# Kernel optimization log

Hardware: AMD Instinct MI355X
Metric: run time of the kernel (lower is better)

The kernel has to match this reference:

```python
import jax, jax.numpy as jnp
import numpy as np

MARGIN = 0.3
IN_FEATURES = 128
NUM_CLASSES = 100
BATCH = 4096


def setup_inputs() -> dict:
    key = jax.random.key(0)
    k1, k2, k3, k4 = jax.random.split(key, 4)
    embeddings = jax.random.normal(k1, (BATCH, IN_FEATURES), dtype=jnp.float32)
    labels = jax.random.randint(k2, (BATCH,), 0, NUM_CLASSES, dtype=jnp.int64)
    # nn.Linear params (kaiming-uniform-ish scale)
    bound = 1.0 / np.sqrt(IN_FEATURES)
    fc_w = jax.random.uniform(k3, (NUM_CLASSES, IN_FEATURES), jnp.float32, -bound, bound)
    fc_b = jax.random.uniform(k4, (NUM_CLASSES,), jnp.float32, -bound, bound)
    return {"embeddings": embeddings, "labels": labels, "fc_w": fc_w, "fc_b": fc_b}


def _triplet_hard(emb, labels, margin):
    # pairwise squared euclidean distances: ||a||^2 + ||b||^2 - 2 a.b
    sq = jnp.sum(emb * emb, axis=1)  # [B]
    d2 = sq[:, None] + sq[None, :] - 2.0 * (emb @ emb.T)
    dist = jnp.sqrt(jnp.clip(d2, 1e-12))  # [B, B]
    same = labels[:, None] == labels[None, :]  # [B, B] (diag True, as in torch)
    neg_inf = jnp.float32(-jnp.inf)
    pos_inf = jnp.float32(jnp.inf)
    ap = jnp.max(jnp.where(same, dist, neg_inf), axis=1)  # hardest positive
    an = jnp.min(jnp.where(same, pos_inf, dist), axis=1)  # hardest negative
    # MarginRankingLoss(target=1): mean(relu(-(an - ap) + margin))
    return jnp.mean(jax.nn.relu(ap - an + margin))


def _cross_entropy(logits, labels):
    logp = jax.nn.log_softmax(logits, axis=-1)
    return -jnp.mean(jnp.take_along_axis(logp, labels[:, None], axis=1)[:, 0])


def reference(embeddings, labels, fc_w, fc_b):
    logits = embeddings @ fc_w.T + fc_b  # [B, C]
    triplet = _triplet_hard(embeddings, labels, MARGIN)
    ce = _cross_entropy(logits, labels)
    return triplet + ce
```

## Files before the change

kernel.cpp:

```cpp
#include <hip/hip_runtime.h>
#include <math.h>

#define BATCH 4096
#define DIM 128
#define NCLS 100
#define MARGIN 0.3f
#define NTILE 272
#define GRID_MAIN 528

typedef __attribute__((ext_vector_type(8))) short short8;
typedef __attribute__((ext_vector_type(4))) float f32x4;

__device__ __forceinline__ unsigned short f2bf(float f) {
    unsigned int u = __float_as_uint(f);
    unsigned int r = (u + 0x7FFFu + ((u >> 16) & 1u)) >> 16;
    return (unsigned short)r;
}
__device__ __forceinline__ float bf2f(unsigned short b) {
    return __uint_as_float(((unsigned int)b) << 16);
}

#define ENC_MAX_ID 0x80000000u
#define ENC_MIN_ID 0x403FFFFFu
__device__ __forceinline__ unsigned int enc_max(float v) {
    return (__float_as_uint(v) >> 1) | 0x80000000u;
}
__device__ __forceinline__ float dec_max(unsigned int k) {
    return __uint_as_float((k & 0x7FFFFFFFu) << 1);
}
__device__ __forceinline__ unsigned int enc_min(float v) {
    return 0x7FFFFFFFu - (__float_as_uint(v) >> 1);
}
__device__ __forceinline__ float dec_min(unsigned int k) {
    return __uint_as_float((0x7FFFFFFFu - k) << 1);
}


__global__ __launch_bounds__(256) void prep_kernel(
        const float* __restrict__ emb, const float* __restrict__ fcw,
        unsigned short* __restrict__ ebf, float* __restrict__ sq,
        unsigned short* __restrict__ wbf, unsigned int* __restrict__ fanz) {
    int bid = blockIdx.x, tid = threadIdx.x;
    if (bid < 256) {
        int wave = tid >> 6, lane = tid & 63;
        unsigned int* dstg = reinterpret_cast<unsigned int*>(ebf) + bid * 1024;
        #pragma unroll
        for (int r = 0; r < 4; ++r) {
            int rowl = wave * 4 + r;
            int row = bid * 16 + rowl;
            const float2* src = reinterpret_cast<const float2*>(emb + row * DIM);
            float2 xy = src[lane];
            unsigned short b0 = f2bf(xy.x), b1 = f2bf(xy.y);
            float y0 = bf2f(b0), y1 = bf2f(b1);
            dstg[(lane >> 2) * 64 + rowl * 4 + (lane & 3)] =
                ((unsigned int)b1 << 16) | (unsigned int)b0;
            float acc = y0 * y0 + y1 * y1;
            #pragma unroll
            for (int off = 1; off < 64; off <<= 1) acc += __shfl_xor(acc, off, 64);
            if (lane == 0) sq[row] = acc;
        }
    } else {
        int idx = (bid - 256) * 256 + tid;
        for (int k = idx; k < 112 * DIM; k += 512) {
            int cls = k >> 7, d = k & 127;
            int dst = (cls >> 4) * 2048 + (d >> 3) * 128 + (cls & 15) * 8 + (d & 7);
            wbf[dst] = (k < NCLS * DIM) ? f2bf(fcw[k]) : (unsigned short)0;
        }
        for (int w = idx; w < 8194; w += 512)
            fanz[w] = 0;
    }
}

__global__ __launch_bounds__(256) void main_kernel(
        const unsigned short* __restrict__ ebf, const unsigned short* __restrict__ wbf,
        const float* __restrict__ sq, const int* __restrict__ labels,
        const float* __restrict__ fcb,
        unsigned int* __restrict__ maxk, unsigned int* __restrict__ mink,
        float* __restrict__ ce_sum, int* __restrict__ ticket,
        float* __restrict__ out) {
    __shared__ float lg[16][128];
    __shared__ unsigned int colk[512];
    __shared__ unsigned short bstage[2][2048];
    __shared__ int lastFlag;
    int bid = blockIdx.x, tid = threadIdx.x;
    int wave = tid >> 6, lane = tid & 63;
    int lm = lane & 15, lq = lane >> 4;

    if (bid < NTILE) {
        int c = 0, rem = bid;
        while (rem >= 2 * c + 2) { rem -= 2 * c + 2; ++c; }
        int rowgrp = rem;
        int chunk  = c;

        int rbase = rowgrp * 128 + wave * 32;
        const unsigned short* apt = ebf + (rbase >> 4) * 2048 + lane * 8;
        short8 a0 = *reinterpret_cast<const short8*>(apt);
        short8 a1 = *reinterpret_cast<const short8*>(apt + 512);
        short8 a2 = *reinterpret_cast<const short8*>(apt + 1024);
        short8 a3 = *reinterpret_cast<const short8*>(apt + 1536);
        short8 a4 = *reinterpret_cast<const short8*>(apt + 2048);
        short8 a5 = *reinterpret_cast<const short8*>(apt + 2560);
        short8 a6 = *reinterpret_cast<const short8*>(apt + 3072);
        short8 a7 = *reinterpret_cast<const short8*>(apt + 3584);

        int labr[8];
        float sqr[8];
        #pragma unroll
        for (int g = 0; g < 2; ++g)
            #pragma unroll
            for (int r = 0; r < 4; ++r) {
                labr[g * 4 + r] = labels[rbase + g * 16 + lq * 4 + r];
                sqr[g * 4 + r]  = sq[rbase + g * 16 + lq * 4 + r];
            }

        colk[tid] = 0; colk[256 + tid] = 0;

        float rmax[8], rmin[8];
        #pragma unroll
        for (int r = 0; r < 8; ++r) { rmax[r] = -INFINITY; rmin[r] = INFINITY; }

        int cbase = chunk * 256;
        const unsigned short* btile = ebf + (cbase >> 4) * 2048 + wave * 512 + lane * 8;
        uint4 breg = *reinterpret_cast<const uint4*>(btile);

        for (int ct = 0; ct < 16; ++ct) {
            *reinterpret_cast<uint4*>(&bstage[ct & 1][wave * 512 + lane * 8]) = breg;
            if (ct < 15)
                breg = *reinterpret_cast<const uint4*>(btile + (ct + 1) * 2048);
            __syncthreads();

            const unsigned short* bb = &bstage[ct & 1][lane * 8];
            short8 b0 = *reinterpret_cast<const short8*>(bb);
            short8 b1 = *reinterpret_cast<const short8*>(bb + 512);
            short8 b2 = *reinterpret_cast<const short8*>(bb + 1024);
            short8 b3 = *reinterpret_cast<const short8*>(bb + 1536);
            f32x4 c0 = {0.f, 0.f, 0.f, 0.f};
            f32x4 c1 = {0.f, 0.f, 0.f, 0.f};
            c0 = __builtin_amdgcn_mfma_f32_16x16x32_bf16(a0, b0, c0, 0, 0, 0);
            c1 = __builtin_amdgcn_mfma_f32_16x16x32_bf16(a4, b0, c1, 0, 0, 0);
            c0 = __builtin_amdgcn_mfma_f32_16x16x32_bf16(a1, b1, c0, 0, 0, 0);
            c1 = __builtin_amdgcn_mfma_f32_16x16x32_bf16(a5, b1, c1, 0, 0, 0);
            c0 = __builtin_amdgcn_mfma_f32_16x16x32_bf16(a2, b2, c0, 0, 0, 0);
            c1 = __builtin_amdgcn_mfma_f32_16x16x32_bf16(a6, b2, c1, 0, 0, 0);
            c0 = __builtin_amdgcn_mfma_f32_16x16x32_bf16(a3, b3, c0, 0, 0, 0);
            c1 = __builtin_amdgcn_mfma_f32_16x16x32_bf16(a7, b3, c1, 0, 0, 0);

            int col = cbase + ct * 16 + lm;
            float sqc = sq[col];
            int lc = labels[col];
            float cmax = -INFINITY, cmin = INFINITY;
            #pragma unroll
            for (int r = 0; r < 4; ++r) {
                float v0 = fmaxf(fmaf(c0[r], -2.0f, sqc) + sqr[r], 0.f);
                bool s0 = (lc == labr[r]);
                rmax[r] = s0 ? fmaxf(rmax[r], v0) : rmax[r];
                rmin[r] = s0 ? rmin[r] : fminf(rmin[r], v0);
                cmax    = s0 ? fmaxf(cmax, v0) : cmax;
                cmin    = s0 ? cmin : fminf(cmin, v0);
                float v1 = fmaxf(fmaf(c1[r], -2.0f, sqc) + sqr[4 + r], 0.f);
                bool s1 = (lc == labr[4 + r]);
                rmax[4 + r] = s1 ? fmaxf(rmax[4 + r], v1) : rmax[4 + r];
                rmin[4 + r] = s1 ? rmin[4 + r] : fminf(rmin[4 + r], v1);
                cmax        = s1 ? fmaxf(cmax, v1) : cmax;
                cmin        = s1 ? cmin : fminf(cmin, v1);
            }
            cmax = fmaxf(cmax, __shfl_xor(cmax, 16, 64));
            cmax = fmaxf(cmax, __shfl_xor(cmax, 32, 64));
            cmin = fminf(cmin, __shfl_xor(cmin, 16, 64));
            cmin = fminf(cmin, __shfl_xor(cmin, 32, 64));
            if (lq == 0) {
                atomicMax(&colk[ct * 16 + lm], enc_max(fmaxf(cmax, 0.f)));
                atomicMax(&colk[256 + ct * 16 + lm], enc_min(fmaxf(cmin, 0.f)));
            }
        }
        #pragma unroll
        for (int off = 1; off < 16; off <<= 1) {
            #pragma unroll
            for (int r = 0; r < 8; ++r) {
                rmax[r] = fmaxf(rmax[r], __shfl_xor(rmax[r], off, 64));
                rmin[r] = fminf(rmin[r], __shfl_xor(rmin[r], off, 64));
            }
        }
        if (lm == 0) {
            #pragma unroll
            for (int g = 0; g < 2; ++g)
                #pragma unroll
                for (int r = 0; r < 4; ++r) {
                    int row = rbase + g * 16 + lq * 4 + r;
                    unsigned int kx = enc_max(fmaxf(rmax[g * 4 + r], 0.f));
                    unsigned int kn = enc_min(fmaxf(rmin[g * 4 + r], 0.f));
                    if (kx != ENC_MAX_ID)
                        __hip_atomic_fetch_max(&maxk[row], kx,
                                               __ATOMIC_RELAXED, __HIP_MEMORY_SCOPE_AGENT);
                    if (kn != ENC_MIN_ID)
                        __hip_atomic_fetch_max(&mink[row], kn,
                                               __ATOMIC_RELAXED, __HIP_MEMORY_SCOPE_AGENT);
                }
        }
        __syncthreads();
        {
            unsigned int kx = colk[tid], kn = colk[256 + tid];
            int col = cbase + tid;
            if (kx > ENC_MAX_ID)
                __hip_atomic_fetch_max(&maxk[col], kx,
                                       __ATOMIC_RELAXED, __HIP_MEMORY_SCOPE_AGENT);
            if (kn != 0 && kn != ENC_MIN_ID)
                __hip_atomic_fetch_max(&mink[col], kn,
                                       __ATOMIC_RELAXED, __HIP_MEMORY_SCOPE_AGENT);
        }
    } else {
        int R0 = (bid - NTILE) * 16;
        lg[tid >> 4][112 + (tid & 15)] = -INFINITY;

        const unsigned short* apt = ebf + (R0 >> 4) * 2048 + lane * 8;
        short8 a0 = *reinterpret_cast<const short8*>(apt);
        short8 a1 = *reinterpret_cast<const short8*>(apt + 512);
        short8 a2 = *reinterpret_cast<const short8*>(apt + 1024);
        short8 a3 = *reinterpret_cast<const short8*>(apt + 1536);

        for (int t = wave * 2; t < 7 && t < wave * 2 + 2; ++t) {
            int cls = t * 16 + lm;
            const unsigned short* bp = wbf + t * 2048 + lane * 8;
            short8 b0 = *reinterpret_cast<const short8*>(bp);
            short8 b1 = *reinterpret_cast<const short8*>(bp + 512);
            short8 b2 = *reinterpret_cast<const short8*>(bp + 1024);
            short8 b3 = *reinterpret_cast<const short8*>(bp + 1536);
            f32x4 c = {0.f, 0.f, 0.f, 0.f};
            c = __builtin_amdgcn_mfma_f32_16x16x32_bf16(a0, b0, c, 0, 0, 0);
            c = __builtin_amdgcn_mfma_f32_16x16x32_bf16(a1, b1, c, 0, 0, 0);
            c = __builtin_amdgcn_mfma_f32_16x16x32_bf16(a2, b2, c, 0, 0, 0);
            c = __builtin_amdgcn_mfma_f32_16x16x32_bf16(a3, b3, c, 0, 0, 0);
            float bias = (cls < NCLS) ? fcb[cls] : -INFINITY;
            #pragma unroll
            for (int r = 0; r < 4; ++r)
                lg[lq * 4 + r][t * 16 + lm] = c[r] + bias;
        }
        __syncthreads();
        float cacc = 0.f;
        #pragma unroll
        for (int i = 0; i < 4; ++i) {
            int r = wave * 4 + i;
            float x0 = lg[r][lane], x1 = lg[r][lane + 64];
            float m = fmaxf(x0, x1);
            #pragma unroll
            for (int off = 1; off < 64; off <<= 1) m = fmaxf(m, __shfl_xor(m, off, 64));
            float s = expf(x0 - m) + expf(x1 - m);
            #pragma unroll
            for (int off = 1; off < 64; off <<= 1) s += __shfl_xor(s, off, 64);
            if (lane == 0) {
                int lab = labels[R0 + r];
                cacc += (m + logf(s)) - lg[r][lab];
            }
        }
        __syncthreads();
        if (lane == 0) lg[0][wave] = cacc;
        __syncthreads();
        if (tid == 0) {
            float bsum = lg[0][0] + lg[0][1] + lg[0][2] + lg[0][3];
            __hip_atomic_fetch_add(ce_sum, bsum,
                                   __ATOMIC_RELAXED, __HIP_MEMORY_SCOPE_AGENT);
        }
    }

    __syncthreads();
    asm volatile("s_waitcnt vmcnt(0)" ::: "memory");
    if (tid == 0) {
        int old = __hip_atomic_fetch_add(ticket, 1,
                                         __ATOMIC_RELAXED, __HIP_MEMORY_SCOPE_AGENT);
        lastFlag = (old == GRID_MAIN - 1);
    }
    __syncthreads();
    if (lastFlag) {
        float acc = 0.f;
        #pragma unroll
        for (int rr = 0; rr < 16; ++rr) {
            int row = rr * 256 + tid;
            unsigned int kx = __hip_atomic_load(&maxk[row], __ATOMIC_RELAXED,
                                                __HIP_MEMORY_SCOPE_AGENT);
            unsigned int kn = __hip_atomic_load(&mink[row], __ATOMIC_RELAXED,
                                                __HIP_MEMORY_SCOPE_AGENT);
            float ap = sqrtf(fmaxf(dec_max(kx), 1e-12f));
            float an = sqrtf(fmaxf(dec_min(kn), 1e-12f));
            acc += fmaxf(ap - an + MARGIN, 0.f);
        }
        float* red = reinterpret_cast<float*>(lg);
        red[tid] = acc;
        __syncthreads();
        for (int s = 128; s > 0; s >>= 1) {
            if (tid < s) red[tid] += red[tid + s];
            __syncthreads();
        }
        if (tid == 0) {
            float ces = __hip_atomic_load(ce_sum, __ATOMIC_RELAXED,
                                          __HIP_MEMORY_SCOPE_AGENT);
            out[0] = (red[0] + ces) * (1.0f / BATCH);
        }
    }
}

extern "C" void kernel_launch(void* const* d_in, const int* in_sizes, int n_in,
                              void* d_out, int out_size, void* d_ws, size_t ws_size,
                              hipStream_t stream) {
    const float* emb    = (const float*)d_in[0];
    const int*   labels = (const int*)  d_in[1];
    const float* fcw    = (const float*)d_in[2];
    const float* fcb    = (const float*)d_in[3];
    float* out = (float*)d_out;

    char* ws = (char*)d_ws;
    unsigned short* ebf = (unsigned short*)(ws);
    unsigned short* wbf = (unsigned short*)(ws + 1048576);
    float* sq           = (float*)(ws + 1081344);
    char* fan           = ws + 1097728;
    int*   ticket       = (int*)(fan);
    float* ce_sum       = (float*)(fan + 4);
    unsigned int* maxk  = (unsigned int*)(fan + 8);
    unsigned int* mink  = (unsigned int*)(fan + 8 + 16384);

    prep_kernel<<<258, 256, 0, stream>>>(emb, fcw, ebf, sq, wbf,
                                         (unsigned int*)fan);
    main_kernel<<<GRID_MAIN, 256, 0, stream>>>(ebf, wbf, sq, labels, fcb,
                                               maxk, mink, ce_sum, ticket, out);
}
```

Baseline: 93.16 us.

## Compute full distance matrix instead of exploiting symmetry with column reductions

Replaces the lower-triangular tile schedule (272 tiles, with each tile reducing both row and column extrema through shared-memory atomics and global atomics) with a full 32x8 grid of 128x512 tiles that only reduce per-row extrema. This removes the column-reduction shuffles, LDS atomics, extra barrier and per-column global atomics, but doubles the MFMA and distance-epilogue work by computing both halves of the symmetric matrix. Grid size shrinks from 528 to 512 blocks, with each distance block running twice as many column tiles.

```diff
diff --git a/kernel.cpp b/kernel.cpp
--- a/kernel.cpp
+++ b/kernel.cpp
@@ -5,8 +5,7 @@
 #define DIM 128
 #define NCLS 100
 #define MARGIN 0.3f
-#define NTILE 272
-#define GRID_MAIN 528
+#define GRID_MAIN 512
 
 typedef __attribute__((ext_vector_type(8))) short short8;
 typedef __attribute__((ext_vector_type(4))) float f32x4;
@@ -79,18 +78,14 @@
         float* __restrict__ ce_sum, int* __restrict__ ticket,
         float* __restrict__ out) {
     __shared__ float lg[16][128];
-    __shared__ unsigned int colk[512];
     __shared__ unsigned short bstage[2][2048];
     __shared__ int lastFlag;
     int bid = blockIdx.x, tid = threadIdx.x;
     int wave = tid >> 6, lane = tid & 63;
     int lm = lane & 15, lq = lane >> 4;
 
-    if (bid < NTILE) {
-        int c = 0, rem = bid;
-        while (rem >= 2 * c + 2) { rem -= 2 * c + 2; ++c; }
-        int rowgrp = rem;
-        int chunk  = c;
+    if (bid < 256) {
+        int rowgrp = bid >> 3, chunk = bid & 7;
 
         int rbase = rowgrp * 128 + wave * 32;
         const unsigned short* apt = ebf + (rbase >> 4) * 2048 + lane * 8;
@@ -113,19 +108,17 @@
                 sqr[g * 4 + r]  = sq[rbase + g * 16 + lq * 4 + r];
             }
 
-        colk[tid] = 0; colk[256 + tid] = 0;
-
         float rmax[8], rmin[8];
         #pragma unroll
         for (int r = 0; r < 8; ++r) { rmax[r] = -INFINITY; rmin[r] = INFINITY; }
 
-        int cbase = chunk * 256;
+        int cbase = chunk * 512;
         const unsigned short* btile = ebf + (cbase >> 4) * 2048 + wave * 512 + lane * 8;
         uint4 breg = *reinterpret_cast<const uint4*>(btile);
 
-        for (int ct = 0; ct < 16; ++ct) {
+        for (int ct = 0; ct < 32; ++ct) {
             *reinterpret_cast<uint4*>(&bstage[ct & 1][wave * 512 + lane * 8]) = breg;
-            if (ct < 15)
+            if (ct < 31)
                 breg = *reinterpret_cast<const uint4*>(btile + (ct + 1) * 2048);
             __syncthreads();
 
@@ -148,29 +141,16 @@
             int col = cbase + ct * 16 + lm;
             float sqc = sq[col];
             int lc = labels[col];
-            float cmax = -INFINITY, cmin = INFINITY;
             #pragma unroll
             for (int r = 0; r < 4; ++r) {
                 float v0 = fmaxf(fmaf(c0[r], -2.0f, sqc) + sqr[r], 0.f);
                 bool s0 = (lc == labr[r]);
                 rmax[r] = s0 ? fmaxf(rmax[r], v0) : rmax[r];
                 rmin[r] = s0 ? rmin[r] : fminf(rmin[r], v0);
-                cmax    = s0 ? fmaxf(cmax, v0) : cmax;
-                cmin    = s0 ? cmin : fminf(cmin, v0);
                 float v1 = fmaxf(fmaf(c1[r], -2.0f, sqc) + sqr[4 + r], 0.f);
                 bool s1 = (lc == labr[4 + r]);
                 rmax[4 + r] = s1 ? fmaxf(rmax[4 + r], v1) : rmax[4 + r];
                 rmin[4 + r] = s1 ? rmin[4 + r] : fminf(rmin[4 + r], v1);
-                cmax        = s1 ? fmaxf(cmax, v1) : cmax;
-                cmin        = s1 ? cmin : fminf(cmin, v1);
-            }
-            cmax = fmaxf(cmax, __shfl_xor(cmax, 16, 64));
-            cmax = fmaxf(cmax, __shfl_xor(cmax, 32, 64));
-            cmin = fminf(cmin, __shfl_xor(cmin, 16, 64));
-            cmin = fminf(cmin, __shfl_xor(cmin, 32, 64));
-            if (lq == 0) {
-                atomicMax(&colk[ct * 16 + lm], enc_max(fmaxf(cmax, 0.f)));
-                atomicMax(&colk[256 + ct * 16 + lm], enc_min(fmaxf(cmin, 0.f)));
             }
         }
         #pragma unroll
@@ -197,19 +177,8 @@
                                                __ATOMIC_RELAXED, __HIP_MEMORY_SCOPE_AGENT);
                 }
         }
-        __syncthreads();
-        {
-            unsigned int kx = colk[tid], kn = colk[256 + tid];
-            int col = cbase + tid;
-            if (kx > ENC_MAX_ID)
-                __hip_atomic_fetch_max(&maxk[col], kx,
-                                       __ATOMIC_RELAXED, __HIP_MEMORY_SCOPE_AGENT);
-            if (kn != 0 && kn != ENC_MIN_ID)
-                __hip_atomic_fetch_max(&mink[col], kn,
-                                       __ATOMIC_RELAXED, __HIP_MEMORY_SCOPE_AGENT);
-        }
     } else {
-        int R0 = (bid - NTILE) * 16;
+        int R0 = (bid - 256) * 16;
         lg[tid >> 4][112 + (tid & 15)] = -INFINITY;
 
         const unsigned short* apt = ebf + (R0 >> 4) * 2048 + lane * 8;
```

New measurement: 96.39 us. +3.5%, slower.

## Fuse CE blocks into triplet tile blocks and double the B-stage per barrier

Applied to the files above, without the earlier changes.

The grid shrinks from 528 to 272 blocks. The first 256 tile blocks now also run the cross-entropy logits work after their triplet tile, where before 256 separate blocks did it. The triplet loop stages two 16-column B tiles per barrier, which halves the number of __syncthreads and doubles the shared B buffer. This removes separate block launches and barrier overhead, at the cost of serializing CE work behind the tile work and using more LDS per block.

```diff
diff --git a/kernel.cpp b/kernel.cpp
--- a/kernel.cpp
+++ b/kernel.cpp
@@ -6,7 +6,7 @@
 #define NCLS 100
 #define MARGIN 0.3f
 #define NTILE 272
-#define GRID_MAIN 528
+#define GRID_MAIN 272
 
 typedef __attribute__((ext_vector_type(8))) short short8;
 typedef __attribute__((ext_vector_type(4))) float f32x4;
@@ -80,17 +80,16 @@
         float* __restrict__ out) {
     __shared__ float lg[16][128];
     __shared__ unsigned int colk[512];
-    __shared__ unsigned short bstage[2][2048];
+    __shared__ unsigned short bstage[2][4096];
     __shared__ int lastFlag;
     int bid = blockIdx.x, tid = threadIdx.x;
     int wave = tid >> 6, lane = tid & 63;
     int lm = lane & 15, lq = lane >> 4;
 
-    if (bid < NTILE) {
+    {
         int c = 0, rem = bid;
         while (rem >= 2 * c + 2) { rem -= 2 * c + 2; ++c; }
-        int rowgrp = rem;
-        int chunk  = c;
+        int rowgrp = rem, chunk = c;
 
         int rbase = rowgrp * 128 + wave * 32;
         const unsigned short* apt = ebf + (rbase >> 4) * 2048 + lane * 8;
@@ -121,56 +120,64 @@
 
         int cbase = chunk * 256;
         const unsigned short* btile = ebf + (cbase >> 4) * 2048 + wave * 512 + lane * 8;
-        uint4 breg = *reinterpret_cast<const uint4*>(btile);
-
-        for (int ct = 0; ct < 16; ++ct) {
-            *reinterpret_cast<uint4*>(&bstage[ct & 1][wave * 512 + lane * 8]) = breg;
-            if (ct < 15)
-                breg = *reinterpret_cast<const uint4*>(btile + (ct + 1) * 2048);
+        uint4 bregA = *reinterpret_cast<const uint4*>(btile);
+        uint4 bregB = *reinterpret_cast<const uint4*>(btile + 2048);
+
+        for (int it = 0; it < 8; ++it) {
+            *reinterpret_cast<uint4*>(&bstage[it & 1][wave * 512 + lane * 8]) = bregA;
+            *reinterpret_cast<uint4*>(&bstage[it & 1][2048 + wave * 512 + lane * 8]) = bregB;
+            if (it < 7) {
+                bregA = *reinterpret_cast<const uint4*>(btile + (2 * it + 2) * 2048);
+                bregB = *reinterpret_cast<const uint4*>(btile + (2 * it + 3) * 2048);
+            }
             __syncthreads();
 
-            const unsigned short* bb = &bstage[ct & 1][lane * 8];
-            short8 b0 = *reinterpret_cast<const short8*>(bb);
-            short8 b1 = *reinterpret_cast<const short8*>(bb + 512);
-            short8 b2 = *reinterpret_cast<const short8*>(bb + 1024);
-            short8 b3 = *reinterpret_cast<const short8*>(bb + 1536);
-            f32x4 c0 = {0.f, 0.f, 0.f, 0.f};
-            f32x4 c1 = {0.f, 0.f, 0.f, 0.f};
-            c0 = __builtin_amdgcn_mfma_f32_16x16x32_bf16(a0, b0, c0, 0, 0, 0);
-            c1 = __builtin_amdgcn_mfma_f32_16x16x32_bf16(a4, b0, c1, 0, 0, 0);
-            c0 = __builtin_amdgcn_mfma_f32_16x16x32_bf16(a1, b1, c0, 0, 0, 0);
-            c1 = __builtin_amdgcn_mfma_f32_16x16x32_bf16(a5, b1, c1, 0, 0, 0);
-            c0 = __builtin_amdgcn_mfma_f32_16x16x32_bf16(a2, b2, c0, 0, 0, 0);
-            c1 = __builtin_amdgcn_mfma_f32_16x16x32_bf16(a6, b2, c1, 0, 0, 0);
-            c0 = __builtin_amdgcn_mfma_f32_16x16x32_bf16(a3, b3, c0, 0, 0, 0);
-            c1 = __builtin_amdgcn_mfma_f32_16x16x32_bf16(a7, b3, c1, 0, 0, 0);
-
-            int col = cbase + ct * 16 + lm;
-            float sqc = sq[col];
-            int lc = labels[col];
-            float cmax = -INFINITY, cmin = INFINITY;
-            #pragma unroll
-            for (int r = 0; r < 4; ++r) {
-                float v0 = fmaxf(fmaf(c0[r], -2.0f, sqc) + sqr[r], 0.f);
-                bool s0 = (lc == labr[r]);
-                rmax[r] = s0 ? fmaxf(rmax[r], v0) : rmax[r];
-                rmin[r] = s0 ? rmin[r] : fminf(rmin[r], v0);
-                cmax    = s0 ? fmaxf(cmax, v0) : cmax;
-                cmin    = s0 ? cmin : fminf(cmin, v0);
-                float v1 = fmaxf(fmaf(c1[r], -2.0f, sqc) + sqr[4 + r], 0.f);
-                bool s1 = (lc == labr[4 + r]);
-                rmax[4 + r] = s1 ? fmaxf(rmax[4 + r], v1) : rmax[4 + r];
-                rmin[4 + r] = s1 ? rmin[4 + r] : fminf(rmin[4 + r], v1);
-                cmax        = s1 ? fmaxf(cmax, v1) : cmax;
-                cmin        = s1 ? cmin : fminf(cmin, v1);
-            }
-            cmax = fmaxf(cmax, __shfl_xor(cmax, 16, 64));
-            cmax = fmaxf(cmax, __shfl_xor(cmax, 32, 64));
-            cmin = fminf(cmin, __shfl_xor(cmin, 16, 64));
-            cmin = fminf(cmin, __shfl_xor(cmin, 32, 64));
-            if (lq == 0) {
-                atomicMax(&colk[ct * 16 + lm], enc_max(fmaxf(cmax, 0.f)));
-                atomicMax(&colk[256 + ct * 16 + lm], enc_min(fmaxf(cmin, 0.f)));
+            #pragma unroll
+            for (int k = 0; k < 2; ++k) {
+                int ct = it * 2 + k;
+                const unsigned short* bb = &bstage[it & 1][k * 2048 + lane * 8];
+                short8 b0 = *reinterpret_cast<const short8*>(bb);
+                short8 b1 = *reinterpret_cast<const short8*>(bb + 512);
+                short8 b2 = *reinterpret_cast<const short8*>(bb + 1024);
+                short8 b3 = *reinterpret_cast<const short8*>(bb + 1536);
+                f32x4 c0 = {0.f, 0.f, 0.f, 0.f};
+                f32x4 c1 = {0.f, 0.f, 0.f, 0.f};
+                c0 = __builtin_amdgcn_mfma_f32_16x16x32_bf16(a0, b0, c0, 0, 0, 0);
+                c1 = __builtin_amdgcn_mfma_f32_16x16x32_bf16(a4, b0, c1, 0, 0, 0);
+                c0 = __builtin_amdgcn_mfma_f32_16x16x32_bf16(a1, b1, c0, 0, 0, 0);
+                c1 = __builtin_amdgcn_mfma_f32_16x16x32_bf16(a5, b1, c1, 0, 0, 0);
+                c0 = __builtin_amdgcn_mfma_f32_16x16x32_bf16(a2, b2, c0, 0, 0, 0);
+                c1 = __builtin_amdgcn_mfma_f32_16x16x32_bf16(a6, b2, c1, 0, 0, 0);
+                c0 = __builtin_amdgcn_mfma_f32_16x16x32_bf16(a3, b3, c0, 0, 0, 0);
+                c1 = __builtin_amdgcn_mfma_f32_16x16x32_bf16(a7, b3, c1, 0, 0, 0);
+
+                int col = cbase + ct * 16 + lm;
+                float sqc = sq[col];
+                int lc = labels[col];
+                float cmax = -INFINITY, cmin = INFINITY;
+                #pragma unroll
+                for (int r = 0; r < 4; ++r) {
+                    float v0 = fmaxf(fmaf(c0[r], -2.0f, sqc) + sqr[r], 0.f);
+                    bool s0 = (lc == labr[r]);
+                    rmax[r] = s0 ? fmaxf(rmax[r], v0) : rmax[r];
+                    rmin[r] = s0 ? rmin[r] : fminf(rmin[r], v0);
+                    cmax    = s0 ? fmaxf(cmax, v0) : cmax;
+                    cmin    = s0 ? cmin : fminf(cmin, v0);
+                    float v1 = fmaxf(fmaf(c1[r], -2.0f, sqc) + sqr[4 + r], 0.f);
+                    bool s1 = (lc == labr[4 + r]);
+                    rmax[4 + r] = s1 ? fmaxf(rmax[4 + r], v1) : rmax[4 + r];
+                    rmin[4 + r] = s1 ? rmin[4 + r] : fminf(rmin[4 + r], v1);
+                    cmax        = s1 ? fmaxf(cmax, v1) : cmax;
+                    cmin        = s1 ? cmin : fminf(cmin, v1);
+                }
+                cmax = fmaxf(cmax, __shfl_xor(cmax, 16, 64));
+                cmax = fmaxf(cmax, __shfl_xor(cmax, 32, 64));
+                cmin = fminf(cmin, __shfl_xor(cmin, 16, 64));
+                cmin = fminf(cmin, __shfl_xor(cmin, 32, 64));
+                if (lq == 0) {
+                    atomicMax(&colk[ct * 16 + lm], enc_max(fmaxf(cmax, 0.f)));
+                    atomicMax(&colk[256 + ct * 16 + lm], enc_min(fmaxf(cmin, 0.f)));
+                }
             }
         }
         #pragma unroll
@@ -208,8 +215,10 @@
                 __hip_atomic_fetch_max(&mink[col], kn,
                                        __ATOMIC_RELAXED, __HIP_MEMORY_SCOPE_AGENT);
         }
-    } else {
-        int R0 = (bid - NTILE) * 16;
+    }
+
+    if (bid < 256) {
+        int R0 = bid * 16;
         lg[tid >> 4][112 + (tid & 15)] = -INFINITY;
 
         const unsigned short* apt = ebf + (R0 >> 4) * 2048 + lane * 8;
```

Result: slower. 95.47 us (+2.5%).
